# Kernel optimization log

Hardware: AMD Instinct MI355X
Metric: run time of the kernel (lower is better)

## Reference

```python
import jax, jax.numpy as jnp
import numpy as np

N_NODES = 100000
N_EDGES = 1600000
N_GRAPHS = 64


def setup_inputs() -> dict:
    key = jax.random.key(0)
    ks = jax.random.split(key, 10)
    x = jax.random.normal(ks[0], (N_NODES, 2), jnp.float32)
    edge_index = jax.random.randint(ks[1], (2, N_EDGES), 0, N_NODES, dtype=jnp.int64)
    batch_index = jnp.sort(jax.random.randint(ks[2], (N_NODES,), 0, N_GRAPHS, dtype=jnp.int64))

    def glorot(k, shape):
        return jax.random.normal(k, shape, jnp.float32) * jnp.sqrt(2.0 / (shape[0] + shape[1]))

    return {
        "x": x,
        "edge_index": edge_index,
        "batch_index": batch_index,
        "W1": glorot(ks[3], (2, 8)),   "b1": jnp.zeros((8,), jnp.float32),
        "W2": glorot(ks[4], (8, 32)),  "b2": jnp.zeros((32,), jnp.float32),
        "W3": glorot(ks[5], (32, 128)),"b3": jnp.zeros((128,), jnp.float32),
        "Wl": glorot(ks[6], (128, 3)), "bl": jnp.zeros((3,), jnp.float32),
    }


def _gcn_conv(x, W, b, src, dst, norm, n):
    # GCNConv: linear transform, then normalized scatter-add aggregation, then bias.
    h = x @ W                                     # [N, out]
    msg = h[src] * norm[:, None]                  # [E', out] gather + scale
    agg = jax.ops.segment_sum(msg, dst, num_segments=n)
    return agg + b


def reference(x, edge_index, batch_index, W1, b1, W2, b2, W3, b3, Wl, bl):
    n = x.shape[0]
    loop = jnp.arange(n, dtype=edge_index.dtype)
    src = jnp.concatenate([edge_index[0], loop])  # add self-loops (GCNConv default)
    dst = jnp.concatenate([edge_index[1], loop])
    # symmetric normalization D^{-1/2} (A+I) D^{-1/2}
    deg = jax.ops.segment_sum(jnp.ones_like(dst, dtype=x.dtype), dst, num_segments=n)
    dis = jnp.where(deg > 0, jax.lax.rsqrt(jnp.maximum(deg, 1.0)), 0.0)
    norm = dis[src] * dis[dst]

    h = jax.nn.relu(_gcn_conv(x, W1, b1, src, dst, norm, n))
    h = jax.nn.relu(_gcn_conv(h, W2, b2, src, dst, norm, n))  # dropout is identity in eval
    h = _gcn_conv(h, W3, b3, src, dst, norm, n)               # [N, 128]
    pooled = jax.ops.segment_max(h, batch_index, num_segments=N_GRAPHS)  # global_max_pool
    logits = pooled @ Wl + bl                                  # [G, 3]
    return jax.nn.log_softmax(logits, axis=1)
```

## Files before the change

### kernel.cpp

```cpp
#include <hip/hip_runtime.h>
#include <hip/hip_fp16.h>


#define BSHIFT 9
#define BSZ 512
#define P2_TILE 2048
#define CAP 16384
#define SRCMASK 0x1FFFF
#define NB3 32

__device__ __forceinline__ unsigned fenc(float x) {
  unsigned b = __float_as_uint(x);
  return (b & 0x80000000u) ? ~b : (b | 0x80000000u);
}
__device__ __forceinline__ float fdec(unsigned k) {
  return (k & 0x80000000u) ? __uint_as_float(k ^ 0x80000000u)
                           : __uint_as_float(~k);
}
__device__ __forceinline__ unsigned pack2(float a, float b) {
  __half2 h = __floats2half2_rn(a, b);
  return *reinterpret_cast<unsigned*>(&h);
}
__device__ __forceinline__ float2 unpack2(unsigned u) {
  __half2 h = *reinterpret_cast<__half2*>(&u);
  return __half22float2(h);
}


__global__ __launch_bounds__(256) void p2_partition_kernel(
    const int* __restrict__ src, const int* __restrict__ dst,
    int* __restrict__ bucketCount, unsigned* __restrict__ part, int E) {
  __shared__ int hist[256];
  __shared__ int lbase[256];
  __shared__ int gbase[256];
  __shared__ int cur[256];
  __shared__ unsigned sbuf[P2_TILE];
  __shared__ unsigned abuf[P2_TILE];
  int t = threadIdx.x;
  int e0 = blockIdx.x * P2_TILE;
  int cnt = min(P2_TILE, E - e0);

  hist[t] = 0;
  __syncthreads();

  int myb[P2_TILE / 256];
  unsigned myp[P2_TILE / 256];
#pragma unroll
  for (int k = 0; k < P2_TILE / 256; ++k) {
    int i = t + k * 256;
    if (i < cnt) {
      int e = e0 + i;
      int d = dst[e];
      int b = d >> BSHIFT;
      myb[k] = b;
      myp[k] = ((unsigned)(d & (BSZ - 1)) << 17) | (unsigned)src[e];
      atomicAdd(&hist[b], 1);
    } else {
      myb[k] = -1;
      myp[k] = 0;
    }
  }
  __syncthreads();

  int v = hist[t];
  lbase[t] = v;
  __syncthreads();
  for (int o = 1; o < 256; o <<= 1) {
    int u = (t >= o) ? lbase[t - o] : 0;
    __syncthreads();
    lbase[t] += u;
    __syncthreads();
  }
  int excl = lbase[t] - v;
  __syncthreads();
  lbase[t] = excl;
  if (v > 0) gbase[t] = atomicAdd(&bucketCount[t], v);
  cur[t] = 0;
  __syncthreads();

#pragma unroll
  for (int k = 0; k < P2_TILE / 256; ++k) {
    int b = myb[k];
    if (b >= 0) {
      int pos = atomicAdd(&cur[b], 1);
      int li = lbase[b] + pos;
      sbuf[li] = myp[k];
      abuf[li] = (unsigned)(b * CAP + gbase[b] + pos);
    }
  }
  __syncthreads();

#pragma unroll
  for (int k = 0; k < P2_TILE / 256; ++k) {
    int i = t + k * 256;
    if (i < cnt) part[abuf[i]] = sbuf[i];
  }
}

__global__ __launch_bounds__(256) void scan_kernel(const int* __restrict__ bucketCount,
                                                   int* __restrict__ bucketBase, int B) {
  __shared__ int s[256];
  int t = threadIdx.x;
  int v = (t < B) ? bucketCount[t] : 0;
  s[t] = v;
  __syncthreads();
  for (int o = 1; o < 256; o <<= 1) {
    int u = (t >= o) ? s[t - o] : 0;
    __syncthreads();
    s[t] += u;
    __syncthreads();
  }
  bucketBase[t] = s[t] - v;
}

__global__ __launch_bounds__(512) void p3_build_kernel(
    const unsigned* __restrict__ part, const int* __restrict__ bucketCount,
    const int* __restrict__ bucketBase,
    const float* __restrict__ x, unsigned* __restrict__ xsh,
    float* __restrict__ dis, int* __restrict__ rp, unsigned* __restrict__ csr,
    int N, int B, int E) {
  __shared__ int hist[BSZ];
  __shared__ int scn[BSZ];
  int b = blockIdx.x, t = threadIdx.x;
  const unsigned* reg = part + (size_t)b * CAP;
  int cnt = bucketCount[b];
  int wbase = bucketBase[b];

  hist[t] = 0;
  __syncthreads();
  for (int i = t; i < cnt; i += BSZ) atomicAdd(&hist[reg[i] >> 17], 1);
  __syncthreads();

  int v = hist[t];
  scn[t] = v;
  __syncthreads();
  for (int o = 1; o < BSZ; o <<= 1) {
    int u = (t >= o) ? scn[t - o] : 0;
    __syncthreads();
    scn[t] += u;
    __syncthreads();
  }
  int excl = scn[t] - v;

  int n = (b << BSHIFT) + t;
  if (n < N) {
    float dn = rsqrtf((float)v + 1.0f);
    dis[n] = dn;
    rp[n] = wbase + excl;
    float2 xn = *reinterpret_cast<const float2*>(x + 2 * (size_t)n);
    xsh[n] = pack2(dn * xn.x, dn * xn.y);
  }
  if (b == B - 1 && t == 0) rp[N] = E;

  hist[t] = excl;
  __syncthreads();
  for (int i = t; i < cnt; i += BSZ) {
    unsigned p = reg[i];
    int pos = atomicAdd(&hist[p >> 17], 1);
    csr[wbase + pos] = p & SRCMASK;
  }
}


__global__ __launch_bounds__(256) void layer1_kernel(
    const int* __restrict__ rp, const unsigned* __restrict__ csr, const float* __restrict__ dis,
    const unsigned* __restrict__ xsh, const float* __restrict__ W1, const float* __restrict__ b1,
    uint4* __restrict__ h1h, int N) {
  __shared__ float sW[16];
  __shared__ float sb[8];
  int t = threadIdx.x;
  if (t < 16) sW[t] = W1[t];
  if (t < 8) sb[t] = b1[t];
  __syncthreads();
  int n = blockIdx.x * blockDim.x + t;
  if (n >= N) return;
  float2 a = unpack2(xsh[n]);
  int j0 = rp[n], j1 = rp[n + 1];
#pragma unroll 4
  for (int j = j0; j < j1; ++j) {
    const float2 v = unpack2(xsh[csr[j]]);
    a.x += v.x;
    a.y += v.y;
  }
  float dn = dis[n];
  float ax = dn * a.x, ay = dn * a.y;
  uint4 pk;
  unsigned* pw = &pk.x;
#pragma unroll
  for (int fc = 0; fc < 4; ++fc) {
    float e0 = dn * fmaxf(ax * sW[fc * 2 + 0] + ay * sW[8 + fc * 2 + 0] + sb[fc * 2 + 0], 0.f);
    float e1 = dn * fmaxf(ax * sW[fc * 2 + 1] + ay * sW[8 + fc * 2 + 1] + sb[fc * 2 + 1], 0.f);
    pw[fc] = pack2(e0, e1);
  }
  h1h[n] = pk;
}

__global__ __launch_bounds__(256) void layer2_kernel(
    const int* __restrict__ rp, const unsigned* __restrict__ csr, const float* __restrict__ dis,
    const uint4* __restrict__ h1h, const float* __restrict__ W2, const float* __restrict__ b2,
    __half* __restrict__ h2h, int N) {
  __shared__ float sW[256];
  __shared__ float sb[32];
  int t = threadIdx.x;
  sW[t] = W2[t];
  if (t < 32) sb[t] = b2[t];
  __syncthreads();
  int n = blockIdx.x * blockDim.x + t;
  if (n >= N) return;
  float acc[8];
  {
    uint4 sv = h1h[n];
    float2 f0 = unpack2(sv.x), f1 = unpack2(sv.y), f2 = unpack2(sv.z), f3 = unpack2(sv.w);
    acc[0] = f0.x; acc[1] = f0.y; acc[2] = f1.x; acc[3] = f1.y;
    acc[4] = f2.x; acc[5] = f2.y; acc[6] = f3.x; acc[7] = f3.y;
  }
  int j0 = rp[n], j1 = rp[n + 1];
#pragma unroll 4
  for (int j = j0; j < j1; ++j) {
    uint4 v = h1h[csr[j]];
    float2 g0 = unpack2(v.x), g1 = unpack2(v.y), g2 = unpack2(v.z), g3 = unpack2(v.w);
    acc[0] += g0.x; acc[1] += g0.y; acc[2] += g1.x; acc[3] += g1.y;
    acc[4] += g2.x; acc[5] += g2.y; acc[6] += g3.x; acc[7] += g3.y;
  }
  float dn = dis[n];
#pragma unroll
  for (int k = 0; k < 8; ++k) acc[k] *= dn;
  uint4 pk[4];
  unsigned* pw = &pk[0].x;
#pragma unroll
  for (int fc = 0; fc < 8; ++fc) {
    float4 o;
    o.x = sb[fc * 4 + 0]; o.y = sb[fc * 4 + 1]; o.z = sb[fc * 4 + 2]; o.w = sb[fc * 4 + 3];
#pragma unroll
    for (int k = 0; k < 8; ++k) {
      const float4 w = *reinterpret_cast<const float4*>(&sW[k * 32 + fc * 4]);
      float a = acc[k];
      o.x += a * w.x; o.y += a * w.y; o.z += a * w.z; o.w += a * w.w;
    }
    o.x = dn * fmaxf(o.x, 0.f);
    o.y = dn * fmaxf(o.y, 0.f);
    o.z = dn * fmaxf(o.z, 0.f);
    o.w = dn * fmaxf(o.w, 0.f);
    pw[fc * 2 + 0] = pack2(o.x, o.y);
    pw[fc * 2 + 1] = pack2(o.z, o.w);
  }
  uint4* dst16 = reinterpret_cast<uint4*>(h2h + (size_t)n * 32);
  dst16[0] = pk[0];
  dst16[1] = pk[1];
  dst16[2] = pk[2];
  dst16[3] = pk[3];
}

__global__ __launch_bounds__(128) void layer3_pool_kernel(
    const int* __restrict__ rp, const unsigned* __restrict__ csr, const float* __restrict__ dis,
    const __half* __restrict__ h2h, const float* __restrict__ W3, const float* __restrict__ b3,
    const int* __restrict__ batch, unsigned* __restrict__ pooled, int N) {
  __shared__ float rows[NB3][32];
  __shared__ float dnv[NB3];
  int t = threadIdx.x;
  int gi = t >> 2;
  int q = t & 3;

  int n0 = blockIdx.x * NB3;
  int m = min(NB3, N - n0);

  if (t < m) dnv[t] = dis[n0 + t];

  if (gi < m) {
    int n = n0 + gi;
    uint4 sv = *reinterpret_cast<const uint4*>(h2h + (size_t)n * 32 + q * 8);
    float2 f0 = unpack2(sv.x), f1 = unpack2(sv.y), f2 = unpack2(sv.z), f3 = unpack2(sv.w);
    float acc[8] = {f0.x, f0.y, f1.x, f1.y, f2.x, f2.y, f3.x, f3.y};
    int j0 = rp[n], j1 = rp[n + 1];
#pragma unroll 4
    for (int j = j0; j < j1; ++j) {
      int s = csr[j];
      uint4 v = *reinterpret_cast<const uint4*>(h2h + (size_t)s * 32 + q * 8);
      float2 g0 = unpack2(v.x), g1 = unpack2(v.y), g2 = unpack2(v.z), g3 = unpack2(v.w);
      acc[0] += g0.x; acc[1] += g0.y; acc[2] += g1.x; acc[3] += g1.y;
      acc[4] += g2.x; acc[5] += g2.y; acc[6] += g3.x; acc[7] += g3.y;
    }
#pragma unroll
    for (int i = 0; i < 8; ++i) rows[gi][q * 8 + i] = acc[i];
  }
  __syncthreads();

  float Wreg[32];
#pragma unroll
  for (int k = 0; k < 32; ++k) Wreg[k] = W3[k * 128 + t];
  float bb = b3[t];

  int curg = batch[n0];
  float runmax = -INFINITY;
  for (int r = 0; r < m; ++r) {
    int g = batch[n0 + r];
    if (g != curg) {
      atomicMax(&pooled[(size_t)curg * 128 + t], fenc(runmax));
      runmax = -INFINITY;
      curg = g;
    }
    float acc = 0.f;
#pragma unroll
    for (int k = 0; k < 32; ++k) acc += rows[r][k] * Wreg[k];
    runmax = fmaxf(runmax, dnv[r] * acc + bb);
  }
  atomicMax(&pooled[(size_t)curg * 128 + t], fenc(runmax));
}

__global__ __launch_bounds__(128) void head_kernel(
    const unsigned* __restrict__ pooled, const float* __restrict__ Wl,
    const float* __restrict__ bl, float* __restrict__ out, int G) {
  int g = blockIdx.x;
  int t = threadIdx.x;
  float p = fdec(pooled[(size_t)g * 128 + t]);
  __shared__ float red[128];
  __shared__ float sj[3];
  for (int j = 0; j < 3; ++j) {
    red[t] = p * Wl[t * 3 + j];
    __syncthreads();
    for (int k = 64; k > 0; k >>= 1) {
      if (t < k) red[t] += red[t + k];
      __syncthreads();
    }
    if (t == 0) sj[j] = red[0];
    __syncthreads();
  }
  if (t == 0) {
    float l0 = sj[0] + bl[0], l1 = sj[1] + bl[1], l2 = sj[2] + bl[2];
    float m = fmaxf(l0, fmaxf(l1, l2));
    float lse = logf(expf(l0 - m) + expf(l1 - m) + expf(l2 - m));
    out[g * 3 + 0] = l0 - m - lse;
    out[g * 3 + 1] = l1 - m - lse;
    out[g * 3 + 2] = l2 - m - lse;
  }
}

extern "C" void kernel_launch(void* const* d_in, const int* in_sizes, int n_in,
                              void* d_out, int out_size, void* d_ws, size_t ws_size,
                              hipStream_t stream) {
  const float* x = (const float*)d_in[0];
  const int* ei = (const int*)d_in[1];
  const int* batch = (const int*)d_in[2];
  const float* W1 = (const float*)d_in[3];
  const float* b1 = (const float*)d_in[4];
  const float* W2 = (const float*)d_in[5];
  const float* b2 = (const float*)d_in[6];
  const float* W3 = (const float*)d_in[7];
  const float* b3 = (const float*)d_in[8];
  const float* Wl = (const float*)d_in[9];
  const float* bl = (const float*)d_in[10];
  float* out = (float*)d_out;

  const int N = in_sizes[0] / 2;
  const int E = in_sizes[1] / 2;
  const int G = out_size / 3;

  const int* src = ei;
  const int* dstp = ei + E;

  const int B = (N + BSZ - 1) / BSZ;

  size_t NP = ((size_t)N + 256) & ~(size_t)255;
  size_t EP = ((size_t)E + 255) & ~(size_t)255;

  float* dis = (float*)d_ws;
  int* rp = (int*)d_ws + NP;
  unsigned* csr = (unsigned*)(rp + NP);
  unsigned* part = (unsigned*)(csr + EP);
  int* ctrl = (int*)(part + (size_t)256 * CAP);
  int* bucketCount = ctrl;
  unsigned* pooled = (unsigned*)(ctrl + 256);
  int* bucketBase = (int*)(pooled + (size_t)G * 128);
  float* arena = (float*)(bucketBase + 256);

  unsigned* xsh = (unsigned*)arena;
  uint4* h1h = (uint4*)(arena + (size_t)N);
  __half* h2h = (__half*)(arena + (size_t)5 * N);

  const int BS = 256;
  auto cdiv = [](long long a, long long b) { return (int)((a + b - 1) / b); };

  hipMemsetAsync(ctrl, 0, (256 + (size_t)G * 128) * 4, stream);
  p2_partition_kernel<<<cdiv(E, P2_TILE), 256, 0, stream>>>(src, dstp, bucketCount, part, E);
  scan_kernel<<<1, 256, 0, stream>>>(bucketCount, bucketBase, B);
  p3_build_kernel<<<B, BSZ, 0, stream>>>(part, bucketCount, bucketBase, x, xsh, dis, rp, csr, N, B, E);

  layer1_kernel<<<cdiv(N, BS), BS, 0, stream>>>(rp, csr, dis, xsh, W1, b1, h1h, N);
  layer2_kernel<<<cdiv(N, BS), BS, 0, stream>>>(rp, csr, dis, h1h, W2, b2, h2h, N);
  layer3_pool_kernel<<<cdiv(N, NB3), 128, 0, stream>>>(rp, csr, dis, h2h, W3, b3, batch, pooled, N);

  head_kernel<<<G, 128, 0, stream>>>(pooled, Wl, bl, out, G);
}
```

Baseline: 119.0 us.

## Fold bucket scan into CSR build and split layer-2 edges across two threads

Removes the separate single-block scan kernel launch: each p3_build block now recomputes the prefix sum of bucket counts in shared memory. Layer 2 now assigns two threads per node, each gathering alternate neighbours, combining partial sums with a lane shuffle, then each computing half of the 32 output features. This doubles parallelism on the latency-bound gather and shortens per-thread dependency chains, at the cost of redundant scans in every build block and twice as many threads. The early return for n >= N happens before the shuffle, but it is applied to both lanes of a pair together, so the pairing stays consistent.

```diff
diff --git a/kernel.cpp b/kernel.cpp
--- a/kernel.cpp
+++ b/kernel.cpp
@@ -97,34 +97,27 @@
   }
 }
 
-__global__ __launch_bounds__(256) void scan_kernel(const int* __restrict__ bucketCount,
-                                                   int* __restrict__ bucketBase, int B) {
-  __shared__ int s[256];
-  int t = threadIdx.x;
-  int v = (t < B) ? bucketCount[t] : 0;
-  s[t] = v;
-  __syncthreads();
-  for (int o = 1; o < 256; o <<= 1) {
-    int u = (t >= o) ? s[t - o] : 0;
-    __syncthreads();
-    s[t] += u;
-    __syncthreads();
-  }
-  bucketBase[t] = s[t] - v;
-}
-
 __global__ __launch_bounds__(512) void p3_build_kernel(
     const unsigned* __restrict__ part, const int* __restrict__ bucketCount,
-    const int* __restrict__ bucketBase,
     const float* __restrict__ x, unsigned* __restrict__ xsh,
     float* __restrict__ dis, int* __restrict__ rp, unsigned* __restrict__ csr,
     int N, int B, int E) {
   __shared__ int hist[BSZ];
   __shared__ int scn[BSZ];
+  __shared__ int sb[256];
   int b = blockIdx.x, t = threadIdx.x;
   const unsigned* reg = part + (size_t)b * CAP;
   int cnt = bucketCount[b];
-  int wbase = bucketBase[b];
+
+  if (t < 256) sb[t] = (t < B) ? bucketCount[t] : 0;
+  __syncthreads();
+  for (int o = 1; o < 256; o <<= 1) {
+    int u = (t < 256 && t >= o) ? sb[t - o] : 0;
+    __syncthreads();
+    if (t < 256) sb[t] += u;
+    __syncthreads();
+  }
+  int wbase = sb[b] - cnt;
 
   hist[t] = 0;
   __syncthreads();
@@ -205,10 +198,12 @@
   sW[t] = W2[t];
   if (t < 32) sb[t] = b2[t];
   __syncthreads();
-  int n = blockIdx.x * blockDim.x + t;
+  int tid = blockIdx.x * blockDim.x + t;
+  int n = tid >> 1;
   if (n >= N) return;
-  float acc[8];
-  {
+  int half = tid & 1;
+  float acc[8] = {0.f, 0.f, 0.f, 0.f, 0.f, 0.f, 0.f, 0.f};
+  if (half == 0) {
     uint4 sv = h1h[n];
     float2 f0 = unpack2(sv.x), f1 = unpack2(sv.y), f2 = unpack2(sv.z), f3 = unpack2(sv.w);
     acc[0] = f0.x; acc[1] = f0.y; acc[2] = f1.x; acc[3] = f1.y;
@@ -216,19 +211,22 @@
   }
   int j0 = rp[n], j1 = rp[n + 1];
 #pragma unroll 4
-  for (int j = j0; j < j1; ++j) {
+  for (int j = j0 + half; j < j1; j += 2) {
     uint4 v = h1h[csr[j]];
     float2 g0 = unpack2(v.x), g1 = unpack2(v.y), g2 = unpack2(v.z), g3 = unpack2(v.w);
     acc[0] += g0.x; acc[1] += g0.y; acc[2] += g1.x; acc[3] += g1.y;
     acc[4] += g2.x; acc[5] += g2.y; acc[6] += g3.x; acc[7] += g3.y;
   }
+#pragma unroll
+  for (int k = 0; k < 8; ++k) acc[k] += __shfl_xor(acc[k], 1);
   float dn = dis[n];
 #pragma unroll
   for (int k = 0; k < 8; ++k) acc[k] *= dn;
-  uint4 pk[4];
+  uint4 pk[2];
   unsigned* pw = &pk[0].x;
 #pragma unroll
-  for (int fc = 0; fc < 8; ++fc) {
+  for (int fc2 = 0; fc2 < 4; ++fc2) {
+    int fc = half * 4 + fc2;
     float4 o;
     o.x = sb[fc * 4 + 0]; o.y = sb[fc * 4 + 1]; o.z = sb[fc * 4 + 2]; o.w = sb[fc * 4 + 3];
 #pragma unroll
@@ -241,14 +239,12 @@
     o.y = dn * fmaxf(o.y, 0.f);
     o.z = dn * fmaxf(o.z, 0.f);
     o.w = dn * fmaxf(o.w, 0.f);
-    pw[fc * 2 + 0] = pack2(o.x, o.y);
-    pw[fc * 2 + 1] = pack2(o.z, o.w);
+    pw[fc2 * 2 + 0] = pack2(o.x, o.y);
+    pw[fc2 * 2 + 1] = pack2(o.z, o.w);
   }
   uint4* dst16 = reinterpret_cast<uint4*>(h2h + (size_t)n * 32);
-  dst16[0] = pk[0];
-  dst16[1] = pk[1];
-  dst16[2] = pk[2];
-  dst16[3] = pk[3];
+  dst16[half * 2 + 0] = pk[0];
+  dst16[half * 2 + 1] = pk[1];
 }
 
 __global__ __launch_bounds__(128) void layer3_pool_kernel(
@@ -370,8 +366,7 @@
   int* ctrl = (int*)(part + (size_t)256 * CAP);
   int* bucketCount = ctrl;
   unsigned* pooled = (unsigned*)(ctrl + 256);
-  int* bucketBase = (int*)(pooled + (size_t)G * 128);
-  float* arena = (float*)(bucketBase + 256);
+  float* arena = (float*)(pooled + (size_t)G * 128);
 
   unsigned* xsh = (unsigned*)arena;
   uint4* h1h = (uint4*)(arena + (size_t)N);
@@ -382,11 +377,10 @@
 
   hipMemsetAsync(ctrl, 0, (256 + (size_t)G * 128) * 4, stream);
   p2_partition_kernel<<<cdiv(E, P2_TILE), 256, 0, stream>>>(src, dstp, bucketCount, part, E);
-  scan_kernel<<<1, 256, 0, stream>>>(bucketCount, bucketBase, B);
-  p3_build_kernel<<<B, BSZ, 0, stream>>>(part, bucketCount, bucketBase, x, xsh, dis, rp, csr, N, B, E);
+  p3_build_kernel<<<B, BSZ, 0, stream>>>(part, bucketCount, x, xsh, dis, rp, csr, N, B, E);
 
   layer1_kernel<<<cdiv(N, BS), BS, 0, stream>>>(rp, csr, dis, xsh, W1, b1, h1h, N);
-  layer2_kernel<<<cdiv(N, BS), BS, 0, stream>>>(rp, csr, dis, h1h, W2, b2, h2h, N);
+  layer2_kernel<<<cdiv((long long)N * 2, BS), BS, 0, stream>>>(rp, csr, dis, h1h, W2, b2, h2h, N);
   layer3_pool_kernel<<<cdiv(N, NB3), 128, 0, stream>>>(rp, csr, dis, h2h, W3, b3, batch, pooled, N);
 
   head_kernel<<<G, 128, 0, stream>>>(pooled, Wl, bl, out, G);
```

Result: no change. 118.3 us (-0.6%).
